# Optimization experiments

Hardware: AMD Instinct MI355X
Metric: run time of the kernel (lower is better)

## Reference

```python
import jax, jax.numpy as jnp
import numpy as np

B = 4            # batch size (coords[:,0].max()+1 in the original)
C = 64           # NUM_BEV_FEATURES
NX, NY, NZ = 432, 496, 1
P_PER = 16000    # pillars per sample per bin
N_BINS = 3       # intersweep_sequence_length


def _make_coords(seed):
    # unique BEV cells per sample: strided modular arange (stride coprime with NX*NY)
    stride = 9973
    cells = (np.arange(P_PER, dtype=np.int64)[None, :] * stride + 17 * seed + 31 * np.arange(B)[:, None]) % (NX * NY)
    y = (cells // NX).reshape(-1)
    x = (cells % NX).reshape(-1)
    b = np.repeat(np.arange(B, dtype=np.int64), P_PER)
    z = np.zeros_like(b)
    return jnp.asarray(np.stack([b, z, y, x], axis=1), dtype=jnp.int32)  # [B*P_PER, 4]


def setup_inputs() -> dict:
    key = jax.random.key(0)
    inp = {}
    for i in range(N_BINS):
        key, kf = jax.random.split(key)
        inp[f"pillar_features_bin_{i}"] = jax.random.normal(kf, (B * P_PER, C), dtype=jnp.float32)
        inp[f"voxel_coords_bin_{i}"] = _make_coords(i)
    return inp


def _scatter_bin(pillars, coords):
    # coords layout: [batch, z, y, x]; per-sample flat index = z + y*nx + x (nz==1)
    c = coords.astype(jnp.int32)
    flat = c[:, 0] * (NY * NX) + c[:, 1] + c[:, 2] * NX + c[:, 3]  # batch-offset flattened index
    canvas = jnp.zeros((B * NY * NX, C), dtype=pillars.dtype).at[flat].set(pillars)
    return canvas.reshape(B, NY, NX, C).transpose(0, 3, 1, 2)  # [B, C, NY, NX]


def reference(pillar_features_bin_0, voxel_coords_bin_0,
              pillar_features_bin_1, voxel_coords_bin_1,
              pillar_features_bin_2, voxel_coords_bin_2):
    out0 = _scatter_bin(pillar_features_bin_0, voxel_coords_bin_0)
    out1 = _scatter_bin(pillar_features_bin_1, voxel_coords_bin_1)
    out2 = _scatter_bin(pillar_features_bin_2, voxel_coords_bin_2)
    return (out0, out1, out2)
```

## Files before the change

### kernel.cpp

```cpp
#include <hip/hip_runtime.h>

#define NX_ 432
#define NY_ 496
#define C_  64
#define B_  4
#define CELLS_ (NX_ * NY_)
#define PLANE_ ((size_t)CELLS_)
#define BATCH_STRIDE_ ((size_t)C_ * CELLS_)
#define BIN_STRIDE_   ((size_t)B_ * C_ * CELLS_)
#define MAP_BIN_ ((size_t)B_ * CELLS_)

#define SPLITS_ 16
#define SPLIT_CELLS_ (CELLS_ / SPLITS_)

typedef float vfloat4 __attribute__((ext_vector_type(4)));
typedef int   vint4   __attribute__((ext_vector_type(4)));

__global__ __launch_bounds__(256) void scatter_idx_kernel(
    const int* __restrict__ coords0,
    const int* __restrict__ coords1,
    const int* __restrict__ coords2,
    int* __restrict__ map, int npil)
{
    const int bin = blockIdx.y;
    const int p = blockIdx.x * 256 + threadIdx.x;
    if (p >= npil) return;
    const int* coords = (bin == 0) ? coords0 : (bin == 1) ? coords1 : coords2;
    vint4 c = ((const vint4*)coords)[p];
    size_t idx = (size_t)bin * MAP_BIN_ + (size_t)c.x * CELLS_ + c.y + c.z * NX_ + c.w;
    map[idx] = p;
}

__global__ __launch_bounds__(256) void gather_kernel(
    const float* __restrict__ pf0,
    const float* __restrict__ pf1,
    const float* __restrict__ pf2,
    const int* __restrict__ map,
    float* __restrict__ out)
{
    const int split = blockIdx.x;
    const int c4    = blockIdx.y;
    const int bb    = blockIdx.z;
    const int bin = bb >> 2;
    const int b   = bb & 3;

    const float* __restrict__ pf = (bin == 0) ? pf0 : (bin == 1) ? pf1 : pf2;
    const float* __restrict__ pfc = pf + c4 * 4;

    const int* mbase = map + (size_t)bin * MAP_BIN_ + (size_t)b * CELLS_
                           + (size_t)split * SPLIT_CELLS_;
    float* obase = out + (size_t)bin * BIN_STRIDE_ + (size_t)b * BATCH_STRIDE_
                       + (size_t)(c4 * 4) * PLANE_ + (size_t)split * SPLIT_CELLS_;

    for (int base = threadIdx.x * 4; base < SPLIT_CELLS_; base += 1024) {
        vint4 idx = *(const vint4*)(mbase + base);
        const bool v0 = idx.x >= 0, v1 = idx.y >= 0, v2 = idx.z >= 0, v3 = idx.w >= 0;

        vfloat4 a0 = *(const vfloat4*)(pfc + (size_t)(v0 ? idx.x : 0) * C_);
        vfloat4 a1 = *(const vfloat4*)(pfc + (size_t)(v1 ? idx.y : 0) * C_);
        vfloat4 a2 = *(const vfloat4*)(pfc + (size_t)(v2 ? idx.z : 0) * C_);
        vfloat4 a3 = *(const vfloat4*)(pfc + (size_t)(v3 ? idx.w : 0) * C_);

        a0 = v0 ? a0 : (vfloat4)0.0f;
        a1 = v1 ? a1 : (vfloat4)0.0f;
        a2 = v2 ? a2 : (vfloat4)0.0f;
        a3 = v3 ? a3 : (vfloat4)0.0f;

        vfloat4 w0 = {a0.x, a1.x, a2.x, a3.x};
        vfloat4 w1 = {a0.y, a1.y, a2.y, a3.y};
        vfloat4 w2 = {a0.z, a1.z, a2.z, a3.z};
        vfloat4 w3 = {a0.w, a1.w, a2.w, a3.w};

        __builtin_nontemporal_store(w0, (vfloat4*)(obase + 0 * PLANE_ + base));
        __builtin_nontemporal_store(w1, (vfloat4*)(obase + 1 * PLANE_ + base));
        __builtin_nontemporal_store(w2, (vfloat4*)(obase + 2 * PLANE_ + base));
        __builtin_nontemporal_store(w3, (vfloat4*)(obase + 3 * PLANE_ + base));
    }
}

extern "C" void kernel_launch(void* const* d_in, const int* in_sizes, int n_in,
                              void* d_out, int out_size, void* d_ws, size_t ws_size,
                              hipStream_t stream) {
    const float* pf0 = (const float*)d_in[0];
    const int*   co0 = (const int*)d_in[1];
    const float* pf1 = (const float*)d_in[2];
    const int*   co1 = (const int*)d_in[3];
    const float* pf2 = (const float*)d_in[4];
    const int*   co2 = (const int*)d_in[5];
    float* out = (float*)d_out;

    const int npil = in_sizes[1] / 4;

    int* map = (int*)d_ws;
    const size_t map_bytes = 3 * MAP_BIN_ * sizeof(int);

    (void)hipMemsetAsync(map, 0xFF, map_bytes, stream);

    dim3 g1((npil + 255) / 256, 3, 1);
    scatter_idx_kernel<<<g1, 256, 0, stream>>>(co0, co1, co2, map, npil);

    dim3 g2(SPLITS_, 16, 12);
    gather_kernel<<<g2, 256, 0, stream>>>(pf0, pf1, pf2, map, out);
}
```

Before: 729.1 us.

## Process 32 channels per block to reuse map indices across channel planes

```diff
diff --git a/kernel.cpp b/kernel.cpp
--- a/kernel.cpp
+++ b/kernel.cpp
@@ -10,8 +10,8 @@
 #define BIN_STRIDE_   ((size_t)B_ * C_ * CELLS_)
 #define MAP_BIN_ ((size_t)B_ * CELLS_)
 
-#define SPLITS_ 16
-#define SPLIT_CELLS_ (CELLS_ / SPLITS_)
+#define SPLITS_ 48
+#define SPAN_ (CELLS_ / SPLITS_)
 
 typedef float vfloat4 __attribute__((ext_vector_type(4)));
 typedef int   vint4   __attribute__((ext_vector_type(4)));
@@ -39,42 +39,52 @@
     float* __restrict__ out)
 {
     const int split = blockIdx.x;
-    const int c4    = blockIdx.y;
+    const int half  = blockIdx.y;
     const int bb    = blockIdx.z;
     const int bin = bb >> 2;
     const int b   = bb & 3;
 
     const float* __restrict__ pf = (bin == 0) ? pf0 : (bin == 1) ? pf1 : pf2;
-    const float* __restrict__ pfc = pf + c4 * 4;
+    const float* __restrict__ pfh = pf + half * 32;
 
     const int* mbase = map + (size_t)bin * MAP_BIN_ + (size_t)b * CELLS_
-                           + (size_t)split * SPLIT_CELLS_;
+                           + (size_t)split * SPAN_;
     float* obase = out + (size_t)bin * BIN_STRIDE_ + (size_t)b * BATCH_STRIDE_
-                       + (size_t)(c4 * 4) * PLANE_ + (size_t)split * SPLIT_CELLS_;
+                       + (size_t)(half * 32) * PLANE_ + (size_t)split * SPAN_;
 
-    for (int base = threadIdx.x * 4; base < SPLIT_CELLS_; base += 1024) {
+    for (int base = threadIdx.x * 4; base < SPAN_; base += 1024) {
         vint4 idx = *(const vint4*)(mbase + base);
         const bool v0 = idx.x >= 0, v1 = idx.y >= 0, v2 = idx.z >= 0, v3 = idx.w >= 0;
 
-        vfloat4 a0 = *(const vfloat4*)(pfc + (size_t)(v0 ? idx.x : 0) * C_);
-        vfloat4 a1 = *(const vfloat4*)(pfc + (size_t)(v1 ? idx.y : 0) * C_);
-        vfloat4 a2 = *(const vfloat4*)(pfc + (size_t)(v2 ? idx.z : 0) * C_);
-        vfloat4 a3 = *(const vfloat4*)(pfc + (size_t)(v3 ? idx.w : 0) * C_);
+        const vfloat4* r0 = (const vfloat4*)(pfh + (size_t)(v0 ? idx.x : 0) * C_);
+        const vfloat4* r1 = (const vfloat4*)(pfh + (size_t)(v1 ? idx.y : 0) * C_);
+        const vfloat4* r2 = (const vfloat4*)(pfh + (size_t)(v2 ? idx.z : 0) * C_);
+        const vfloat4* r3 = (const vfloat4*)(pfh + (size_t)(v3 ? idx.w : 0) * C_);
 
-        a0 = v0 ? a0 : (vfloat4)0.0f;
-        a1 = v1 ? a1 : (vfloat4)0.0f;
-        a2 = v2 ? a2 : (vfloat4)0.0f;
-        a3 = v3 ? a3 : (vfloat4)0.0f;
+        float* o = obase + base;
 
-        vfloat4 w0 = {a0.x, a1.x, a2.x, a3.x};
-        vfloat4 w1 = {a0.y, a1.y, a2.y, a3.y};
-        vfloat4 w2 = {a0.z, a1.z, a2.z, a3.z};
-        vfloat4 w3 = {a0.w, a1.w, a2.w, a3.w};
+        #pragma unroll 2
+        for (int c4 = 0; c4 < 8; ++c4) {
+            vfloat4 a0 = r0[c4];
+            vfloat4 a1 = r1[c4];
+            vfloat4 a2 = r2[c4];
+            vfloat4 a3 = r3[c4];
+            a0 = v0 ? a0 : (vfloat4)0.0f;
+            a1 = v1 ? a1 : (vfloat4)0.0f;
+            a2 = v2 ? a2 : (vfloat4)0.0f;
+            a3 = v3 ? a3 : (vfloat4)0.0f;
 
-        __builtin_nontemporal_store(w0, (vfloat4*)(obase + 0 * PLANE_ + base));
-        __builtin_nontemporal_store(w1, (vfloat4*)(obase + 1 * PLANE_ + base));
-        __builtin_nontemporal_store(w2, (vfloat4*)(obase + 2 * PLANE_ + base));
-        __builtin_nontemporal_store(w3, (vfloat4*)(obase + 3 * PLANE_ + base));
+            vfloat4 w0 = {a0.x, a1.x, a2.x, a3.x};
+            vfloat4 w1 = {a0.y, a1.y, a2.y, a3.y};
+            vfloat4 w2 = {a0.z, a1.z, a2.z, a3.z};
+            vfloat4 w3 = {a0.w, a1.w, a2.w, a3.w};
+
+            float* oc = o + (size_t)(c4 * 4) * PLANE_;
+            __builtin_nontemporal_store(w0, (vfloat4*)(oc));
+            __builtin_nontemporal_store(w1, (vfloat4*)(oc + PLANE_));
+            __builtin_nontemporal_store(w2, (vfloat4*)(oc + 2 * PLANE_));
+            __builtin_nontemporal_store(w3, (vfloat4*)(oc + 3 * PLANE_));
+        }
     }
 }
 
@@ -99,6 +109,6 @@
     dim3 g1((npil + 255) / 256, 3, 1);
     scatter_idx_kernel<<<g1, 256, 0, stream>>>(co0, co1, co2, map, npil);
 
-    dim3 g2(SPLITS_, 16, 12);
+    dim3 g2(SPLITS_, 2, 12);
     gather_kernel<<<g2, 256, 0, stream>>>(pf0, pf1, pf2, map, out);
 }
```

After: 718.0 us. Within noise of the previous version (-1.5%).
